# Optimization experiments

Hardware: AMD Instinct MI355X
Metric: run time of the kernel (lower is better)

## Reference

```python
import jax, jax.numpy as jnp
import numpy as np

B, L, D, V1, V2, V3 = 512, 48, 256, 512, 512, 64


def setup_inputs() -> dict:
    key = jax.random.key(0)
    ks = jax.random.split(key, 20)
    def w(k, shape, fan_in):
        return jax.random.normal(k, shape, dtype=jnp.float32) / np.sqrt(fan_in)
    inp = {
        'x1': jax.random.normal(ks[0], (B, L, V1), dtype=jnp.float32),
        'x2': jax.random.normal(ks[1], (B, L, V2), dtype=jnp.float32),
        's': jax.random.normal(ks[2], (B, V3), dtype=jnp.float32),
        'w_e1': w(ks[3], (D, V1), V1), 'b_e1': jnp.zeros((D,), jnp.float32),
        'w_e2': w(ks[4], (D, V2), V2), 'b_e2': jnp.zeros((D,), jnp.float32),
        'w_s': w(ks[5], (D, V3), V3), 'b_s': jnp.zeros((D,), jnp.float32),
        'w_x': w(ks[6], (1, D), D),                      # mlp_for_x, no bias
        'w_h': w(ks[7], (L, D), D), 'b_h': w(ks[8], (L,), D),  # mlp_for_hidden
        'w_ih': w(ks[9], (3 * D, D), D), 'w_hh': w(ks[10], (3 * D, D), D),
        'b_ih': w(ks[11], (3 * D,), D), 'b_hh': w(ks[12], (3 * D,), D),
        'w_out': w(ks[13], (1, D), D), 'b_out': jnp.zeros((1,), jnp.float32),
    }
    return inp


def _gru_cell(x, h, w_ih, w_hh, b_ih, b_hh):
    # torch GRUCell: gates ordered r, z, n
    gi = x @ w_ih.T + b_ih
    gh = h @ w_hh.T + b_hh
    i_r, i_z, i_n = jnp.split(gi, 3, axis=-1)
    h_r, h_z, h_n = jnp.split(gh, 3, axis=-1)
    r = jax.nn.sigmoid(i_r + h_r)
    z = jax.nn.sigmoid(i_z + h_z)
    n = jnp.tanh(i_n + r * h_n)
    return (1.0 - z) * n + z * h


def reference(x1, x2, s, w_e1, b_e1, w_e2, b_e2, w_s, b_s, w_x, w_h, b_h,
              w_ih, w_hh, b_ih, b_hh, w_out, b_out):
    x1e = jax.nn.relu(jnp.einsum('blv,dv->bld', x1, w_e1) + b_e1)
    x2e = jax.nn.relu(jnp.einsum('blv,dv->bld', x2, w_e2) + b_e2)
    se = s @ w_s.T + b_s                      # [B, D]
    x = x1e + x2e                             # [B, L, D]
    # prefix[:, i] = sum_{j < i} x2e[:, j, 0]  (the torch.where zero test)
    cums = jnp.cumsum(x2e[:, :, 0], axis=1)
    prefix = jnp.concatenate([jnp.zeros((B, 1), x.dtype), cums[:, :-1]], axis=1)  # [B, L]
    idx = jnp.arange(L)

    def step(h, inputs):
        i, pref = inputs                       # i: scalar step, pref: [B]
        le = (idx <= i).astype(x.dtype)        # keep timesteps 0..i (pad rest with 0)
        ip = x * le[None, :, None]             # input_padded [B, L, D]
        lt = (idx < i)
        cond = (pref == 0.0)[:, None]          # batches with zero history in ch0
        guid = jnp.where(idx[None, :] == i, 1.0,
                         jnp.where(cond & lt[None, :], 1.0, 0.0)).astype(x.dtype)  # [B, L]
        gi = ip * guid[:, :, None]
        t1 = jnp.einsum('bld,d->bl', gi, w_x[0]) + (h @ w_h.T + b_h)  # [B, L]
        a = jax.nn.softmax(t1, axis=1)
        ctx = jnp.einsum('bld,bl->bd', ip, a)
        h2 = _gru_cell(ctx, h, w_ih, w_hh, b_ih, b_hh)
        return h2, None

    h0 = jnp.zeros((B, D), x.dtype)
    hF, _ = jax.lax.scan(step, h0, (idx, prefix.T))
    y = jax.nn.sigmoid((hF + se) @ w_out.T + b_out)  # [B, 1]
    return y
```

## Files before the change

kernel.cpp:

```cpp
#include <hip/hip_runtime.h>
#include <stdint.h>

#define B_ 512
#define L_ 48
#define D_ 256

typedef __attribute__((ext_vector_type(8))) short bf16x8;
typedef __attribute__((ext_vector_type(4))) short bf16x4;
typedef __attribute__((ext_vector_type(4))) float f32x4;
typedef __attribute__((ext_vector_type(4))) int i32x4;

__device__ __forceinline__ short f2bf(float f) {
    union { float f; unsigned u; } v; v.f = f;
    unsigned u = v.u;
    unsigned r = (u + 0x7FFFu + ((u >> 16) & 1u)) >> 16;
    return (short)r;
}
__device__ __forceinline__ float bf2f(short s) {
    union { unsigned u; float f; } v; v.u = ((unsigned)(unsigned short)s) << 16;
    return v.f;
}

__global__ __launch_bounds__(256) void k_prep(const float* __restrict__ w_hh,
                                              const float* __restrict__ w_h,
                                              const float* __restrict__ w_ih,
                                              signed char* __restrict__ W1q,
                                              signed char* __restrict__ W2q,
                                              float* __restrict__ qA,
                                              float* __restrict__ qC) {
    int w = threadIdx.x >> 6, lane = threadIdx.x & 63;
    int R = blockIdx.x * 4 + w;
    if (R >= 1584) return;
    const float* src;
    signed char* dst;
    bool isA = (R < 816);
    if (R < 768)      { src = w_hh + (size_t)R * 256;         dst = W1q + (size_t)R * 256; }
    else if (R < 816) { src = w_h + (size_t)(R - 768) * 256;  dst = W1q + (size_t)R * 256; }
    else              { src = w_ih + (size_t)(R - 816) * 256; dst = W2q + (size_t)(R - 816) * 256; }
    float4 v = *(const float4*)(src + lane * 4);
    float m = fmaxf(fmaxf(fabsf(v.x), fabsf(v.y)), fmaxf(fabsf(v.z), fabsf(v.w)));
    #pragma unroll
    for (int o = 32; o; o >>= 1) m = fmaxf(m, __shfl_xor(m, o));
    float sc = (m > 0.f) ? 127.f / m : 0.f;
    int b0 = __float2int_rn(v.x * sc), b1 = __float2int_rn(v.y * sc);
    int b2 = __float2int_rn(v.z * sc), b3 = __float2int_rn(v.w * sc);
    unsigned word = (unsigned)(b0 & 255) | ((unsigned)(b1 & 255) << 8) |
                    ((unsigned)(b2 & 255) << 16) | ((unsigned)(b3 & 255) << 24);
    ((unsigned*)dst)[lane] = word;
    if (lane == 0) {
        if (isA) qA[R] = m / (127.f * 127.f);
        else     qC[R - 816] = m * 8.f / (127.f * 127.f);
    }
}

__device__ __forceinline__ void gemm_pass(const float* __restrict__ X,
                                          const float* __restrict__ W,
                                          short (*sA)[40], short (*sB)[40],
                                          int m0, int n0, int srow, int sseg,
                                          int mf, int nf, int row16, int kg,
                                          f32x4 (&acc)[2][4]) {
    for (int k0 = 0; k0 < 512; k0 += 32) {
        __syncthreads();
        {
            const float* src = X + (size_t)(m0 + srow) * 512 + k0 + sseg * 8;
            float4 p0 = *(const float4*)(src);
            float4 p1 = *(const float4*)(src + 4);
            bf16x8 v;
            v[0] = f2bf(p0.x); v[1] = f2bf(p0.y); v[2] = f2bf(p0.z); v[3] = f2bf(p0.w);
            v[4] = f2bf(p1.x); v[5] = f2bf(p1.y); v[6] = f2bf(p1.z); v[7] = f2bf(p1.w);
            *(bf16x8*)&sA[srow][sseg * 8] = v;
        }
        {
            const float* src = W + (size_t)(n0 + srow) * 512 + k0 + sseg * 8;
            float4 p0 = *(const float4*)(src);
            float4 p1 = *(const float4*)(src + 4);
            bf16x8 v;
            v[0] = f2bf(p0.x); v[1] = f2bf(p0.y); v[2] = f2bf(p0.z); v[3] = f2bf(p0.w);
            v[4] = f2bf(p1.x); v[5] = f2bf(p1.y); v[6] = f2bf(p1.z); v[7] = f2bf(p1.w);
            *(bf16x8*)&sB[srow][sseg * 8] = v;
        }
        __syncthreads();
        bf16x8 a0 = *(bf16x8*)&sA[(mf + 0) * 16 + row16][kg * 8];
        bf16x8 a1 = *(bf16x8*)&sA[(mf + 1) * 16 + row16][kg * 8];
        #pragma unroll
        for (int j = 0; j < 4; ++j) {
            bf16x8 bv = *(bf16x8*)&sB[(nf + j) * 16 + row16][kg * 8];
            acc[0][j] = __builtin_amdgcn_mfma_f32_16x16x32_bf16(a0, bv, acc[0][j], 0, 0, 0);
            acc[1][j] = __builtin_amdgcn_mfma_f32_16x16x32_bf16(a1, bv, acc[1][j], 0, 0, 0);
        }
    }
}

__global__ __launch_bounds__(512) void k_embed(const float* __restrict__ x1,
                                               const float* __restrict__ x2,
                                               const float* __restrict__ w_e1,
                                               const float* __restrict__ b_e1,
                                               const float* __restrict__ w_e2,
                                               const float* __restrict__ b_e2,
                                               short* __restrict__ xb) {
    __shared__ short sA[128][40];
    __shared__ short sB[128][40];
    int bid = blockIdx.x;
    int mt = bid >> 1, nt = bid & 1;
    int m0 = mt * 128, n0 = nt * 128;
    int tid = threadIdx.x;
    int lane = tid & 63, w = tid >> 6;
    int mf = (w & 3) * 2;
    int nf = (w >> 2) * 4;
    int row16 = lane & 15, kg = lane >> 4;
    int srow = tid >> 2, sseg = tid & 3;

    f32x4 acc[2][4], keep[2][4];
    #pragma unroll
    for (int a = 0; a < 2; ++a)
        #pragma unroll
        for (int j = 0; j < 4; ++j) { acc[a][j] = {0.f, 0.f, 0.f, 0.f}; }

    gemm_pass(x1, w_e1, sA, sB, m0, n0, srow, sseg, mf, nf, row16, kg, acc);
    #pragma unroll
    for (int a = 0; a < 2; ++a)
        #pragma unroll
        for (int j = 0; j < 4; ++j) { keep[a][j] = acc[a][j]; acc[a][j] = {0.f, 0.f, 0.f, 0.f}; }
    gemm_pass(x2, w_e2, sA, sB, m0, n0, srow, sseg, mf, nf, row16, kg, acc);

    #pragma unroll
    for (int a = 0; a < 2; ++a) {
        int mbase = m0 + (mf + a) * 16 + kg * 4;
        #pragma unroll
        for (int j = 0; j < 4; ++j) {
            int n = n0 + (nf + j) * 16 + row16;
            float be1 = b_e1[n], be2 = b_e2[n];
            #pragma unroll
            for (int e = 0; e < 4; ++e) {
                float v1 = fmaxf(keep[a][j][e] + be1, 0.f);
                float v2 = fmaxf(acc[a][j][e] + be2, 0.f);
                xb[(size_t)(mbase + e) * 256 + n] = f2bf(v1 + v2);
            }
        }
    }
}

__global__ __launch_bounds__(256) void k_quant(const short* __restrict__ xb,
                                               signed char* __restrict__ xq,
                                               float* __restrict__ xs) {
    int w = threadIdx.x >> 6, lane = threadIdx.x & 63;
    int row = blockIdx.x * 4 + w;
    const short* src = xb + (size_t)row * 256 + lane * 4;
    bf16x4 v = *(const bf16x4*)src;
    float f0 = bf2f(v.x), f1 = bf2f(v.y), f2 = bf2f(v.z), f3 = bf2f(v.w);
    float m = fmaxf(fmaxf(f0, f1), fmaxf(f2, f3));
    #pragma unroll
    for (int o = 32; o; o >>= 1) m = fmaxf(m, __shfl_xor(m, o));
    float sc = (m > 0.f) ? 127.f / m : 0.f;
    int b0 = __float2int_rn(f0 * sc), b1 = __float2int_rn(f1 * sc);
    int b2 = __float2int_rn(f2 * sc), b3 = __float2int_rn(f3 * sc);
    unsigned word = (unsigned)(b0 & 255) | ((unsigned)(b1 & 255) << 8) |
                    ((unsigned)(b2 & 255) << 16) | ((unsigned)(b3 & 255) << 24);
    ((unsigned*)xq)[(size_t)row * 64 + lane] = word;
    if (lane == 0) xs[row] = m / 127.f;
}

__global__ __launch_bounds__(256) void k_aux(const float* __restrict__ x2,
                                             const float* __restrict__ w_e2,
                                             const float* __restrict__ b_e2,
                                             const short* __restrict__ xb,
                                             const float* __restrict__ w_x,
                                             float* __restrict__ c0,
                                             float* __restrict__ xw) {
    int w = threadIdx.x >> 6, lane = threadIdx.x & 63;
    int m = blockIdx.x * 4 + w;
    const float* xr = x2 + (size_t)m * 512 + lane * 8;
    const float* wr = w_e2 + lane * 8;
    float s = 0.f;
    #pragma unroll
    for (int q = 0; q < 8; ++q) s += xr[q] * wr[q];
    #pragma unroll
    for (int o = 32; o; o >>= 1) s += __shfl_xor(s, o);
    float pre = s + b_e2[0];

    float t = 0.f;
    if (lane < 32) {
        const short* xbr = xb + (size_t)m * 256 + lane * 8;
        #pragma unroll
        for (int q = 0; q < 8; ++q) t += bf2f(xbr[q]) * w_x[lane * 8 + q];
    }
    #pragma unroll
    for (int o = 32; o; o >>= 1) t += __shfl_xor(t, o);
    if (lane == 0) { c0[m] = fmaxf(pre, 0.f); xw[m] = t; }
}

__global__ __launch_bounds__(256) void k_aux2(const float* __restrict__ c0,
                                              const float* __restrict__ s_in,
                                              const float* __restrict__ w_s,
                                              const float* __restrict__ b_s,
                                              unsigned long long* __restrict__ condbits,
                                              float* __restrict__ se) {
    __shared__ float sS[64];
    int b = blockIdx.x;
    int t = threadIdx.x;
    if (t < 64) sS[t] = s_in[b * 64 + t];
    __syncthreads();
    float acc = b_s[t];
    const float* wr = w_s + t * 64;
    #pragma unroll 8
    for (int kk = 0; kk < 64; ++kk) acc += sS[kk] * wr[kk];
    se[(size_t)b * 256 + t] = acc;
    if (t == 0) {
        unsigned long long bits = 0;
        bool run = true;
        const float* cr = c0 + (size_t)b * 48;
        for (int i = 0; i < 48; ++i) {
            if (run) bits |= (1ull << i);
            run = run && (cr[i] == 0.0f);
        }
        condbits[b] = bits;
    }
}

__device__ __forceinline__ void mfma4r(const i32x4 (&a)[4], const i32x4 (&b)[4], i32x4& acc) {
    #pragma unroll
    for (int s = 0; s < 4; ++s)
        acc = __builtin_amdgcn_mfma_i32_16x16x64_i8(a[s], b[s], acc, 0, 0, 0);
}

__global__ __launch_bounds__(512, 1) void k_scan(const signed char* __restrict__ W1q,
                                                 const signed char* __restrict__ W2q,
                                                 const float* __restrict__ qAg,
                                                 const float* __restrict__ qCg,
                                                 const float* __restrict__ b_hh,
                                                 const float* __restrict__ b_h,
                                                 const float* __restrict__ b_ih,
                                                 const signed char* __restrict__ xq,
                                                 const float* __restrict__ xs,
                                                 const float* __restrict__ xw,
                                                 const unsigned long long* __restrict__ condbits,
                                                 const float* __restrict__ se,
                                                 const float* __restrict__ w_out,
                                                 const float* __restrict__ b_out,
                                                 float* __restrict__ out) {
    __shared__ signed char lWc[8][3][4096];
    __shared__ signed char lWs[3][4096];
    __shared__ signed char lH8[16][272];
    __shared__ signed char lX8[16][272];
    __shared__ float lS[16][52];
    __shared__ float lXW[2][48], lXS[2][48];
    __shared__ float lbA[816], lqA[816], lbC[768], lqC[768];
    __shared__ float lRed[8][2];
    __shared__ unsigned long long lC[2];

    const int tid = threadIdx.x;
    const int w = tid >> 6, lane = tid & 63;
    const int row16 = lane & 15, kg = lane >> 4;
    const int b0 = blockIdx.x * 2;
    const int g1 = 8 + w;
    const int c0 = w * 16 + row16, c1 = g1 * 16 + row16;
    const int swz = (row16 & 7) << 4;
    const float CS = 127.f / 8.f;
    const int mb = w >> 2;
    const int dimb = ((w & 3) << 6) + lane;

    for (int t = tid; t < 816; t += 512) {
        lbA[t] = (t < 768) ? b_hh[t] : b_h[t - 768];
        lqA[t] = qAg[t];
    }
    for (int t = tid; t < 768; t += 512) { lbC[t] = b_ih[t]; lqC[t] = qCg[t]; }
    if (tid < 96) {
        int m = tid / 48, j = tid - m * 48;
        lXW[m][j] = xw[(size_t)(b0 + m) * 48 + j];
        lXS[m][j] = xs[(size_t)(b0 + m) * 48 + j];
    }
    if (tid < 2) lC[tid] = condbits[b0 + tid];
    for (int t = tid; t < 1088; t += 512) {
        ((int*)lH8)[t] = 0;
        ((int*)lX8)[t] = 0;
    }

    const int fro = row16 * 256 + kg * 16;
    i32x4 wa0[3][4], wa1[3][4], wc0[3][4];
    #pragma unroll
    for (int t = 0; t < 3; ++t) {
        const signed char* p0 = W1q + (size_t)(t * 16 + w) * 4096 + fro;
        const signed char* p1 = W1q + (size_t)(t * 16 + g1) * 4096 + fro;
        const signed char* p2 = W2q + (size_t)(t * 16 + w) * 4096 + fro;
        #pragma unroll
        for (int s = 0; s < 4; ++s) {
            wa0[t][s] = *(const i32x4*)(p0 + s * 64);
            wa1[t][s] = *(const i32x4*)(p1 + s * 64);
            wc0[t][s] = *(const i32x4*)(p2 + s * 64);
        }
    }
    #pragma unroll
    for (int t = 0; t < 3; ++t) {
        const signed char* src = W2q + (size_t)(t * 16 + g1) * 4096 + fro;
        signed char* dst = &lWc[w][t][row16 * 256];
        #pragma unroll
        for (int s = 0; s < 4; ++s)
            *(i32x4*)(dst + ((kg * 16 + s * 64) ^ swz)) = *(const i32x4*)(src + s * 64);
    }
    if (w < 3) {
        const signed char* src = W1q + (size_t)(48 + w) * 4096 + fro;
        signed char* dst = &lWs[w][row16 * 256];
        #pragma unroll
        for (int s = 0; s < 4; ++s)
            *(i32x4*)(dst + ((kg * 16 + s * 64) ^ swz)) = *(const i32x4*)(src + s * 64);
    }
    __syncthreads();

    const signed char* xp = xq + (size_t)(b0 + mb) * 48 * 256 + dimb;

    float h0[2] = {0.f, 0.f};
    float h1[2] = {0.f, 0.f};

    for (int i = 0; i < 48; ++i) {
        i32x4 av[4];
        #pragma unroll
        for (int s = 0; s < 4; ++s) av[s] = *(const i32x4*)(&lH8[row16][0] + kg * 16 + s * 64);
        i32x4 aR0 = {0,0,0,0}, aZ0 = {0,0,0,0}, aN0 = {0,0,0,0};
        i32x4 aR1 = {0,0,0,0}, aZ1 = {0,0,0,0}, aN1 = {0,0,0,0};
        mfma4r(av, wa0[0], aR0); mfma4r(av, wa0[1], aZ0); mfma4r(av, wa0[2], aN0);
        mfma4r(av, wa1[0], aR1); mfma4r(av, wa1[1], aZ1); mfma4r(av, wa1[2], aN1);
        if (w < 3) {
            i32x4 scv = {0,0,0,0};
            #pragma unroll
            for (int s = 0; s < 4; ++s) {
                i32x4 b = *(const i32x4*)(&lWs[w][row16 * 256] + ((kg * 16 + s * 64) ^ swz));
                scv = __builtin_amdgcn_mfma_i32_16x16x64_i8(av[s], b, scv, 0, 0, 0);
            }
            const int n = 768 + w * 16 + row16;
            const float q = lqA[n], bb = lbA[n];
            #pragma unroll
            for (int e = 0; e < 2; ++e) lS[kg * 4 + e][w * 16 + row16] = (float)scv[e] * q + bb;
        }
        __syncthreads();

        float pv;
        {
            float val = -3.0e38f;
            if (lane < 48) {
                val = lS[mb][lane];
                bool cb = (lC[mb] >> i) & 1ull;
                if (lane == i) val += lXW[mb][i];
                else if (cb && lane < i) val += lXW[mb][lane];
            }
            float mx = val;
            #pragma unroll
            for (int o = 32; o; o >>= 1) mx = fmaxf(mx, __shfl_xor(mx, o));
            float ex = (lane < 48) ? __expf(val - mx) : 0.f;
            float sm = ex;
            #pragma unroll
            for (int o = 32; o; o >>= 1) sm += __shfl_xor(sm, o);
            pv = (lane < 48) ? (ex / sm) * lXS[mb][lane] : 0.f;
        }
        {
            float acc = 0.f;
            #pragma unroll 4
            for (int j = 0; j <= i; ++j) {
                float aj = __shfl(pv, j);
                acc += aj * (float)xp[(size_t)j * 256];
            }
            lX8[mb][dimb] = (signed char)__float2int_rn(fminf(fmaxf(acc * CS, -127.f), 127.f));
        }
        __syncthreads();

        i32x4 cv[4];
        #pragma unroll
        for (int s = 0; s < 4; ++s) cv[s] = *(const i32x4*)(&lX8[row16][0] + kg * 16 + s * 64);
        {
            i32x4 cr = {0,0,0,0}, cz = {0,0,0,0}, cn = {0,0,0,0};
            mfma4r(cv, wc0[0], cr); mfma4r(cv, wc0[1], cz); mfma4r(cv, wc0[2], cn);
            #pragma unroll
            for (int e = 0; e < 2; ++e) {
                float gr = (float)aR0[e] * lqA[c0]       + lbA[c0]       + (float)cr[e] * lqC[c0]       + lbC[c0];
                float gz = (float)aZ0[e] * lqA[256 + c0] + lbA[256 + c0] + (float)cz[e] * lqC[256 + c0] + lbC[256 + c0];
                float gh = (float)aN0[e] * lqA[512 + c0] + lbA[512 + c0];
                float gn = (float)cn[e] * lqC[512 + c0]  + lbC[512 + c0];
                float r = 1.f / (1.f + __expf(-gr));
                float z = 1.f / (1.f + __expf(-gz));
                float nn = 1.f - 2.f / (__expf(2.f * (gn + r * gh)) + 1.f);
                float hp = (1.f - z) * nn + z * h0[e];
                h0[e] = hp;
                if (kg == 0)
                    lH8[e][c0] = (signed char)__float2int_rn(fminf(fmaxf(hp, -1.f), 1.f) * 127.f);
            }
        }
        {
            i32x4 cr = {0,0,0,0}, cz = {0,0,0,0}, cn = {0,0,0,0};
            #pragma unroll
            for (int s = 0; s < 4; ++s) {
                int off = (kg * 16 + s * 64) ^ swz;
                i32x4 br = *(const i32x4*)(&lWc[w][0][row16 * 256] + off);
                i32x4 bz = *(const i32x4*)(&lWc[w][1][row16 * 256] + off);
                i32x4 bn = *(const i32x4*)(&lWc[w][2][row16 * 256] + off);
                cr = __builtin_amdgcn_mfma_i32_16x16x64_i8(cv[s], br, cr, 0, 0, 0);
                cz = __builtin_amdgcn_mfma_i32_16x16x64_i8(cv[s], bz, cz, 0, 0, 0);
                cn = __builtin_amdgcn_mfma_i32_16x16x64_i8(cv[s], bn, cn, 0, 0, 0);
            }
            #pragma unroll
            for (int e = 0; e < 2; ++e) {
                float gr = (float)aR1[e] * lqA[c1]       + lbA[c1]       + (float)cr[e] * lqC[c1]       + lbC[c1];
                float gz = (float)aZ1[e] * lqA[256 + c1] + lbA[256 + c1] + (float)cz[e] * lqC[256 + c1] + lbC[256 + c1];
                float gh = (float)aN1[e] * lqA[512 + c1] + lbA[512 + c1];
                float gn = (float)cn[e] * lqC[512 + c1]  + lbC[512 + c1];
                float r = 1.f / (1.f + __expf(-gr));
                float z = 1.f / (1.f + __expf(-gz));
                float nn = 1.f - 2.f / (__expf(2.f * (gn + r * gh)) + 1.f);
                float hp = (1.f - z) * nn + z * h1[e];
                h1[e] = hp;
                if (kg == 0)
                    lH8[e][c1] = (signed char)__float2int_rn(fminf(fmaxf(hp, -1.f), 1.f) * 127.f);
            }
        }
        __syncthreads();
    }

    if (kg == 0) {
        float p[2];
        #pragma unroll
        for (int e = 0; e < 2; ++e) {
            int b = b0 + e;
            p[e] = (h0[e] + se[(size_t)b * 256 + c0]) * w_out[c0]
                 + (h1[e] + se[(size_t)b * 256 + c1]) * w_out[c1];
        }
        #pragma unroll
        for (int o = 1; o < 16; o <<= 1) {
            #pragma unroll
            for (int e = 0; e < 2; ++e) p[e] += __shfl_xor(p[e], o);
        }
        if (row16 == 0) {
            #pragma unroll
            for (int e = 0; e < 2; ++e) lRed[w][e] = p[e];
        }
    }
    __syncthreads();
    if (tid < 2) {
        float sum = 0.f;
        #pragma unroll
        for (int q = 0; q < 8; ++q) sum += lRed[q][tid];
        out[b0 + tid] = 1.f / (1.f + __expf(-(sum + b_out[0])));
    }
}

extern "C" void kernel_launch(void* const* d_in, const int* in_sizes, int n_in,
                              void* d_out, int out_size, void* d_ws, size_t ws_size,
                              hipStream_t stream) {
    const float* x1   = (const float*)d_in[0];
    const float* x2   = (const float*)d_in[1];
    const float* s    = (const float*)d_in[2];
    const float* w_e1 = (const float*)d_in[3];
    const float* b_e1 = (const float*)d_in[4];
    const float* w_e2 = (const float*)d_in[5];
    const float* b_e2 = (const float*)d_in[6];
    const float* w_s  = (const float*)d_in[7];
    const float* b_s  = (const float*)d_in[8];
    const float* w_x  = (const float*)d_in[9];
    const float* w_h  = (const float*)d_in[10];
    const float* b_h  = (const float*)d_in[11];
    const float* w_ih = (const float*)d_in[12];
    const float* w_hh = (const float*)d_in[13];
    const float* b_ih = (const float*)d_in[14];
    const float* b_hh = (const float*)d_in[15];
    const float* w_out = (const float*)d_in[16];
    const float* b_out = (const float*)d_in[17];
    float* out = (float*)d_out;

    char* ws = (char*)d_ws;
    size_t off = 0;
    auto alloc = [&](size_t bytes) -> void* {
        void* p = ws + off;
        off = (off + bytes + 255) & ~(size_t)255;
        return p;
    };
    short* xb = (short*)alloc((size_t)B_ * L_ * D_ * 2);
    signed char* xq = (signed char*)alloc((size_t)B_ * L_ * D_);
    float* xs = (float*)alloc((size_t)B_ * L_ * 4);
    signed char* W1q = (signed char*)alloc(896 * 256);
    signed char* W2q = (signed char*)alloc(768 * 256);
    float* qA = (float*)alloc(816 * 4);
    float* qC = (float*)alloc(768 * 4);
    float* c0 = (float*)alloc((size_t)B_ * L_ * 4);
    float* xw = (float*)alloc((size_t)B_ * L_ * 4);
    unsigned long long* cb = (unsigned long long*)alloc(B_ * 8);
    float* se = (float*)alloc((size_t)B_ * D_ * 4);

    hipLaunchKernelGGL(k_prep, dim3(396), dim3(256), 0, stream,
                       w_hh, w_h, w_ih, W1q, W2q, qA, qC);
    hipLaunchKernelGGL(k_embed, dim3(384), dim3(512), 0, stream,
                       x1, x2, w_e1, b_e1, w_e2, b_e2, xb);
    hipLaunchKernelGGL(k_quant, dim3(6144), dim3(256), 0, stream,
                       xb, xq, xs);
    hipLaunchKernelGGL(k_aux, dim3(6144), dim3(256), 0, stream,
                       x2, w_e2, b_e2, xb, w_x, c0, xw);
    hipLaunchKernelGGL(k_aux2, dim3(512), dim3(256), 0, stream,
                       c0, s, w_s, b_s, cb, se);
    hipLaunchKernelGGL(k_scan, dim3(256), dim3(512), 0, stream,
                       W1q, W2q, qA, qC, b_hh, b_h, b_ih, xq, xs, xw, cb, se,
                       w_out, b_out, out);
}
```

Before: 287.5 us.

## Stage quantized inputs in LDS for the scan and fuse the x·w_x dot into quant

The scan kernel now copies each block's int8 input sequence (2×48×256 bytes) into shared memory once, instead of rereading it from global memory at every step of the context reduction. The softmax weights go through a small shared table rather than per-iteration shuffles. The score MFMA is moved ahead of the gate MFMAs, and the x·w_x dot product is computed inside the quant kernel, so the aux kernel no longer rereads xb. The cost is about 24KB more LDS per block on top of an already large footprint, which could affect occupancy or hit allocation limits.

```diff
diff --git a/kernel.cpp b/kernel.cpp
--- a/kernel.cpp
+++ b/kernel.cpp
@@ -141,32 +141,36 @@
 }
 
 __global__ __launch_bounds__(256) void k_quant(const short* __restrict__ xb,
+                                               const float* __restrict__ w_x,
                                                signed char* __restrict__ xq,
-                                               float* __restrict__ xs) {
+                                               float* __restrict__ xs,
+                                               float* __restrict__ xw) {
     int w = threadIdx.x >> 6, lane = threadIdx.x & 63;
     int row = blockIdx.x * 4 + w;
     const short* src = xb + (size_t)row * 256 + lane * 4;
     bf16x4 v = *(const bf16x4*)src;
     float f0 = bf2f(v.x), f1 = bf2f(v.y), f2 = bf2f(v.z), f3 = bf2f(v.w);
     float m = fmaxf(fmaxf(f0, f1), fmaxf(f2, f3));
-    #pragma unroll
-    for (int o = 32; o; o >>= 1) m = fmaxf(m, __shfl_xor(m, o));
+    float t = f0 * w_x[lane * 4] + f1 * w_x[lane * 4 + 1] +
+              f2 * w_x[lane * 4 + 2] + f3 * w_x[lane * 4 + 3];
+    #pragma unroll
+    for (int o = 32; o; o >>= 1) {
+        m = fmaxf(m, __shfl_xor(m, o));
+        t += __shfl_xor(t, o);
+    }
     float sc = (m > 0.f) ? 127.f / m : 0.f;
     int b0 = __float2int_rn(f0 * sc), b1 = __float2int_rn(f1 * sc);
     int b2 = __float2int_rn(f2 * sc), b3 = __float2int_rn(f3 * sc);
     unsigned word = (unsigned)(b0 & 255) | ((unsigned)(b1 & 255) << 8) |
                     ((unsigned)(b2 & 255) << 16) | ((unsigned)(b3 & 255) << 24);
     ((unsigned*)xq)[(size_t)row * 64 + lane] = word;
-    if (lane == 0) xs[row] = m / 127.f;
+    if (lane == 0) { xs[row] = m / 127.f; xw[row] = t; }
 }
 
 __global__ __launch_bounds__(256) void k_aux(const float* __restrict__ x2,
                                              const float* __restrict__ w_e2,
                                              const float* __restrict__ b_e2,
-                                             const short* __restrict__ xb,
-                                             const float* __restrict__ w_x,
-                                             float* __restrict__ c0,
-                                             float* __restrict__ xw) {
+                                             float* __restrict__ c0) {
     int w = threadIdx.x >> 6, lane = threadIdx.x & 63;
     int m = blockIdx.x * 4 + w;
     const float* xr = x2 + (size_t)m * 512 + lane * 8;
@@ -176,17 +180,7 @@
     for (int q = 0; q < 8; ++q) s += xr[q] * wr[q];
     #pragma unroll
     for (int o = 32; o; o >>= 1) s += __shfl_xor(s, o);
-    float pre = s + b_e2[0];
-
-    float t = 0.f;
-    if (lane < 32) {
-        const short* xbr = xb + (size_t)m * 256 + lane * 8;
-        #pragma unroll
-        for (int q = 0; q < 8; ++q) t += bf2f(xbr[q]) * w_x[lane * 8 + q];
-    }
-    #pragma unroll
-    for (int o = 32; o; o >>= 1) t += __shfl_xor(t, o);
-    if (lane == 0) { c0[m] = fmaxf(pre, 0.f); xw[m] = t; }
+    if (lane == 0) c0[m] = fmaxf(s + b_e2[0], 0.f);
 }
 
 __global__ __launch_bounds__(256) void k_aux2(const float* __restrict__ c0,
@@ -240,9 +234,11 @@
                                                  float* __restrict__ out) {
     __shared__ signed char lWc[8][3][4096];
     __shared__ signed char lWs[3][4096];
+    __shared__ signed char lXq[2 * 48 * 256];
     __shared__ signed char lH8[16][272];
     __shared__ signed char lX8[16][272];
     __shared__ float lS[16][52];
+    __shared__ float lTw[8][49];
     __shared__ float lXW[2][48], lXS[2][48];
     __shared__ float lbA[816], lqA[816], lbC[768], lqC[768];
     __shared__ float lRed[8][2];
@@ -274,6 +270,12 @@
         ((int*)lH8)[t] = 0;
         ((int*)lX8)[t] = 0;
     }
+    {
+        const int4* src = (const int4*)(xq + (size_t)b0 * 48 * 256);
+        int4* dst = (int4*)lXq;
+        #pragma unroll
+        for (int t = 0; t < 3; ++t) dst[tid + t * 512] = src[tid + t * 512];
+    }
 
     const int fro = row16 * 256 + kg * 16;
     i32x4 wa0[3][4], wa1[3][4], wc0[3][4];
@@ -306,7 +308,7 @@
     }
     __syncthreads();
 
-    const signed char* xp = xq + (size_t)(b0 + mb) * 48 * 256 + dimb;
+    const signed char* xl = lXq + mb * 12288 + dimb;
 
     float h0[2] = {0.f, 0.f};
     float h1[2] = {0.f, 0.f};
@@ -315,25 +317,24 @@
         i32x4 av[4];
         #pragma unroll
         for (int s = 0; s < 4; ++s) av[s] = *(const i32x4*)(&lH8[row16][0] + kg * 16 + s * 64);
+        if (w < 3) {
+            i32x4 scv = {0,0,0,0};
+            #pragma unroll
+            for (int s = 0; s < 4; ++s) {
+                i32x4 b = *(const i32x4*)(&lWs[w][row16 * 256] + ((kg * 16 + s * 64) ^ swz));
+                scv = __builtin_amdgcn_mfma_i32_16x16x64_i8(av[s], b, scv, 0, 0, 0);
+            }
+            const int n = 768 + w * 16 + row16;
+            const float q = lqA[n], bb = lbA[n];
+            #pragma unroll
+            for (int e = 0; e < 2; ++e) lS[kg * 4 + e][w * 16 + row16] = (float)scv[e] * q + bb;
+        }
         i32x4 aR0 = {0,0,0,0}, aZ0 = {0,0,0,0}, aN0 = {0,0,0,0};
         i32x4 aR1 = {0,0,0,0}, aZ1 = {0,0,0,0}, aN1 = {0,0,0,0};
         mfma4r(av, wa0[0], aR0); mfma4r(av, wa0[1], aZ0); mfma4r(av, wa0[2], aN0);
         mfma4r(av, wa1[0], aR1); mfma4r(av, wa1[1], aZ1); mfma4r(av, wa1[2], aN1);
-        if (w < 3) {
-            i32x4 scv = {0,0,0,0};
-            #pragma unroll
-            for (int s = 0; s < 4; ++s) {
-                i32x4 b = *(const i32x4*)(&lWs[w][row16 * 256] + ((kg * 16 + s * 64) ^ swz));
-                scv = __builtin_amdgcn_mfma_i32_16x16x64_i8(av[s], b, scv, 0, 0, 0);
-            }
-            const int n = 768 + w * 16 + row16;
-            const float q = lqA[n], bb = lbA[n];
-            #pragma unroll
-            for (int e = 0; e < 2; ++e) lS[kg * 4 + e][w * 16 + row16] = (float)scv[e] * q + bb;
-        }
         __syncthreads();
 
-        float pv;
         {
             float val = -3.0e38f;
             if (lane < 48) {
@@ -349,15 +350,14 @@
             float sm = ex;
             #pragma unroll
             for (int o = 32; o; o >>= 1) sm += __shfl_xor(sm, o);
-            pv = (lane < 48) ? (ex / sm) * lXS[mb][lane] : 0.f;
-        }
-        {
+            if (lane < 48) lTw[w][lane] = (ex / sm) * lXS[mb][lane];
+        }
+        {
+            const float* tw = lTw[w];
             float acc = 0.f;
             #pragma unroll 4
-            for (int j = 0; j <= i; ++j) {
-                float aj = __shfl(pv, j);
-                acc += aj * (float)xp[(size_t)j * 256];
-            }
+            for (int j = 0; j <= i; ++j)
+                acc += tw[j] * (float)xl[j * 256];
             lX8[mb][dimb] = (signed char)__float2int_rn(fminf(fmaxf(acc * CS, -127.f), 127.f));
         }
         __syncthreads();
@@ -487,9 +487,9 @@
     hipLaunchKernelGGL(k_embed, dim3(384), dim3(512), 0, stream,
                        x1, x2, w_e1, b_e1, w_e2, b_e2, xb);
     hipLaunchKernelGGL(k_quant, dim3(6144), dim3(256), 0, stream,
-                       xb, xq, xs);
+                       xb, w_x, xq, xs, xw);
     hipLaunchKernelGGL(k_aux, dim3(6144), dim3(256), 0, stream,
-                       x2, w_e2, b_e2, xb, w_x, c0, xw);
+                       x2, w_e2, b_e2, c0);
     hipLaunchKernelGGL(k_aux2, dim3(512), dim3(256), 0, stream,
                        c0, s, w_s, b_s, cb, se);
     hipLaunchKernelGGL(k_scan, dim3(256), dim3(512), 0, stream,
```

New measurement: 241.6 us. 1.19x faster.
